# Performance work log

Measured on AMD Instinct MI355X. Metric: run time of the kernel, lower is better.

The kernel has to match this reference:

```python
import jax, jax.numpy as jnp
import numpy as np

B, A, H, L = 4096, 4096, 768, 4  # batch, num_atoms, hidden_dim, antecedent_len


def setup_inputs() -> dict:
    key = jax.random.key(0)
    ks = jax.random.split(key, 10)
    s = 0.02
    cls = jax.random.normal(ks[0], (B, H), jnp.float32)
    x_ = jax.random.bernoulli(ks[1], 0.5, (B, A)).astype(jnp.float32)
    gru_w_ih = jax.random.normal(ks[2], (3 * H, H), jnp.float32) * s
    gru_w_hh = jax.random.normal(ks[3], (3 * H, H), jnp.float32) * s
    gru_b_ih = jax.random.normal(ks[4], (3 * H,), jnp.float32) * s
    gru_b_hh = jax.random.normal(ks[5], (3 * H,), jnp.float32) * s
    head_w = jax.random.normal(ks[6], (A, H), jnp.float32) * s
    head_b = jax.random.normal(ks[7], (A,), jnp.float32) * s
    ae_weight = jax.random.normal(ks[8], (A, H), jnp.float32) * s
    return {"cls": cls, "x_": x_, "gru_w_ih": gru_w_ih, "gru_w_hh": gru_w_hh,
            "gru_b_ih": gru_b_ih, "gru_b_hh": gru_b_hh, "head_w": head_w,
            "head_b": head_b, "ae_weight": ae_weight}


def _gru_step(x, h, w_ih, w_hh, b_ih, b_hh):
    # torch GRU gate order: r, z, n
    gi = x @ w_ih.T + b_ih          # [B, 3H]
    gh = h @ w_hh.T + b_hh
    i_r, i_z, i_n = jnp.split(gi, 3, axis=-1)
    h_r, h_z, h_n = jnp.split(gh, 3, axis=-1)
    r = jax.nn.sigmoid(i_r + h_r)
    z = jax.nn.sigmoid(i_z + h_z)
    n = jnp.tanh(i_n + r * h_n)
    return (1.0 - z) * n + z * h


def reference(cls, x_, gru_w_ih, gru_w_hh, gru_b_ih, gru_b_hh, head_w, head_b, ae_weight):
    key = jax.random.key(42)
    mask = x_
    h = jnp.zeros_like(cls)
    cur_input = cls
    max_index = None
    rows = jnp.arange(B)
    probs = []
    for j in range(L):
        h = _gru_step(cur_input, h, gru_w_ih, gru_w_hh, gru_b_ih, gru_b_hh)
        out = h @ head_w.T + head_b  # [B, A]  (dropout = identity in eval)
        # filtered_softmax mask update (mutations persist across steps)
        if j == 0:
            empty = jnp.sum(mask, axis=-1) == 0.0
            mask = mask.at[:, 0].set(jnp.where(empty, 1.0, mask[:, 0]))
        else:
            mask = jnp.where((max_index == 0)[:, None], 0.0, mask)
            mask = mask.at[:, 0].set(1.0)
        logits = jnp.where(mask > 0, out, -jnp.inf)
        # hard gumbel-softmax, tau=1 (straight-through)
        key, sub = jax.random.split(key)
        g = jax.random.gumbel(sub, logits.shape, logits.dtype)
        y_soft = jax.nn.softmax(logits + g, axis=1)
        idx = jnp.argmax(y_soft, axis=1)
        y_hard = jax.nn.one_hot(idx, A, dtype=y_soft.dtype)
        prob = y_hard + y_soft - jax.lax.stop_gradient(y_soft)
        max_index = idx
        # scatter zeros at the selected atom (remove from candidate set)
        mask = mask.at[rows, idx].set(0.0)
        probs.append(prob)
        atom_wsum = prob @ jax.lax.stop_gradient(ae_weight)  # [B, H]
        cur_input = cls + atom_wsum
    return jnp.stack(probs, axis=1)  # [B, L, A]
```

## Files before the change

### kernel.cpp

```cpp
#include <hip/hip_runtime.h>
#include <cstdint>
#include <cstddef>
#include <math.h>


#define KB 4096
#define KA 4096
#define KH 768
#define KL 4

typedef __attribute__((ext_vector_type(8))) short bf16x8;
typedef __attribute__((ext_vector_type(4))) float f32x4;

__host__ __device__ inline unsigned rotl32(unsigned x, int d) {
  return (x << d) | (x >> (32 - d));
}

__host__ __device__ inline void tf2x32(unsigned k0, unsigned k1,
                                       unsigned x0, unsigned x1,
                                       unsigned& o0, unsigned& o1) {
  unsigned ks2 = k0 ^ k1 ^ 0x1BD11BDAu;
  x0 += k0; x1 += k1;
#define TF_R(r) { x0 += x1; x1 = rotl32(x1, (r)); x1 ^= x0; }
  TF_R(13) TF_R(15) TF_R(26) TF_R(6)
  x0 += k1;  x1 += ks2 + 1u;
  TF_R(17) TF_R(29) TF_R(16) TF_R(24)
  x0 += ks2; x1 += k0 + 2u;
  TF_R(13) TF_R(15) TF_R(26) TF_R(6)
  x0 += k0;  x1 += k1 + 3u;
  TF_R(17) TF_R(29) TF_R(16) TF_R(24)
  x0 += k1;  x1 += ks2 + 4u;
  TF_R(13) TF_R(15) TF_R(26) TF_R(6)
  x0 += ks2; x1 += k0 + 5u;
#undef TF_R
  o0 = x0; o1 = x1;
}

__device__ inline ushort f2bf(float f) {
  unsigned u = __float_as_uint(f);
  unsigned r = (u + 0x7fffu + ((u >> 16) & 1u)) >> 16;
  return (ushort)r;
}
__device__ inline float bf2f(ushort h) {
  return __uint_as_float(((unsigned)h) << 16);
}

__device__ inline float gumbel_at(unsigned s0, unsigned s1, unsigned ctr) {
  unsigned o0, o1;
  tf2x32(s0, s1, 0u, ctr, o0, o1);
  unsigned bits = o0 ^ o1;
  float f = __uint_as_float((bits >> 9) | 0x3f800000u) - 1.0f;
  const float TINY = 1.17549435e-38f;
  float u = fmaxf(TINY, f + TINY);
  return -logf(-logf(u));
}

#define GLDS(gp, lp) \
  __builtin_amdgcn_global_load_lds( \
      (const __attribute__((address_space(1))) void*)(gp), \
      (__attribute__((address_space(3))) void*)(lp), 16, 0, 0)

__global__ __launch_bounds__(256, 4) void gemm3_nt(
    const ushort* __restrict__ Ahi, const ushort* __restrict__ Alo,
    const ushort* __restrict__ Bhi, const ushort* __restrict__ Blo,
    float* __restrict__ C, long long ldc) {
  __shared__ ushort smem[4 * 128 * 32];
  const int tid = threadIdx.x;
  const int wave = tid >> 6;
  const int lane = tid & 63;
  const long long bm = (long long)blockIdx.y * 128;
  const long long bn = (long long)blockIdx.x * 128;
  const int wm = (wave & 1) * 64;
  const int wn = (wave >> 1) * 64;

  f32x4 acc[4][4];
#pragma unroll
  for (int i = 0; i < 4; ++i)
#pragma unroll
    for (int j = 0; j < 4; ++j) acc[i][j] = (f32x4){0.f, 0.f, 0.f, 0.f};

  const int r = lane >> 2;
  const int cs = lane & 3;
  const int csrc = cs ^ ((r & 3) ^ ((r >> 2) & 3));
  const int m15 = lane & 15;
  const int kg = (lane >> 4) & 3;
  const int slot = kg ^ ((m15 & 3) ^ ((m15 >> 2) & 3));

  for (int kt = 0; kt < 24; ++kt) {
    const int k0 = kt * 32;
#pragma unroll
    for (int s = 0; s < 2; ++s) {
      const int m0 = wave * 32 + s * 16;
      const long long arow = (bm + m0 + r) * KH + k0 + csrc * 8;
      const long long brow = (bn + m0 + r) * KH + k0 + csrc * 8;
      GLDS(Ahi + arow, &smem[0 * 4096 + m0 * 32]);
      GLDS(Alo + arow, &smem[1 * 4096 + m0 * 32]);
      GLDS(Bhi + brow, &smem[2 * 4096 + m0 * 32]);
      GLDS(Blo + brow, &smem[3 * 4096 + m0 * 32]);
    }
    __syncthreads();
    bf16x8 bh[4], bl[4];
#pragma unroll
    for (int jj = 0; jj < 4; ++jj) {
      const int n = wn + jj * 16 + m15;
      bh[jj] = *(const bf16x8*)&smem[2 * 4096 + n * 32 + slot * 8];
      bl[jj] = *(const bf16x8*)&smem[3 * 4096 + n * 32 + slot * 8];
    }
#pragma unroll
    for (int i = 0; i < 4; ++i) {
      const int m = wm + i * 16 + m15;
      bf16x8 ah = *(const bf16x8*)&smem[0 * 4096 + m * 32 + slot * 8];
      bf16x8 al = *(const bf16x8*)&smem[1 * 4096 + m * 32 + slot * 8];
#pragma unroll
      for (int jj = 0; jj < 4; ++jj) {
        acc[i][jj] = __builtin_amdgcn_mfma_f32_16x16x32_bf16(ah, bh[jj], acc[i][jj], 0, 0, 0);
        acc[i][jj] = __builtin_amdgcn_mfma_f32_16x16x32_bf16(ah, bl[jj], acc[i][jj], 0, 0, 0);
        acc[i][jj] = __builtin_amdgcn_mfma_f32_16x16x32_bf16(al, bh[jj], acc[i][jj], 0, 0, 0);
      }
    }
    __syncthreads();
  }
  const int rq = (lane >> 4) * 4;
#pragma unroll
  for (int i = 0; i < 4; ++i)
#pragma unroll
    for (int j = 0; j < 4; ++j) {
      const long long n = bn + wn + j * 16 + m15;
#pragma unroll
      for (int rg = 0; rg < 4; ++rg) {
        const long long m = bm + wm + i * 16 + rq + rg;
        C[m * ldc + n] = acc[i][j][rg];
      }
    }
}

__global__ __launch_bounds__(256, 4) void gemm_fused(
    const ushort* __restrict__ hHi, const ushort* __restrict__ hLo,
    const ushort* __restrict__ WhhHi, const ushort* __restrict__ WhhLo,
    float* __restrict__ Gh, const ushort* __restrict__ HwHi,
    const float* __restrict__ head_b, ushort* __restrict__ Vbuf, int gh_nb) {
  __shared__ ushort smem[4 * 128 * 32];
  const int tid = threadIdx.x;
  const int wave = tid >> 6;
  const int lane = tid & 63;
  const int bid = blockIdx.x;
  const int wm = (wave & 1) * 64;
  const int wn = (wave >> 1) * 64;
  const int r = lane >> 2;
  const int cs = lane & 3;
  const int csrc = cs ^ ((r & 3) ^ ((r >> 2) & 3));
  const int m15 = lane & 15;
  const int kg = (lane >> 4) & 3;
  const int slot = kg ^ ((m15 & 3) ^ ((m15 >> 2) & 3));

  f32x4 acc[4][4];
#pragma unroll
  for (int i = 0; i < 4; ++i)
#pragma unroll
    for (int j = 0; j < 4; ++j) acc[i][j] = (f32x4){0.f, 0.f, 0.f, 0.f};

  if (bid < gh_nb) {
    const long long bm = (long long)(bid / 18) * 128;
    const long long bn = (long long)(bid % 18) * 128;
    for (int kt = 0; kt < 24; ++kt) {
      const int k0 = kt * 32;
#pragma unroll
      for (int s = 0; s < 2; ++s) {
        const int m0 = wave * 32 + s * 16;
        const long long arow = (bm + m0 + r) * KH + k0 + csrc * 8;
        const long long brow = (bn + m0 + r) * KH + k0 + csrc * 8;
        GLDS(hHi + arow, &smem[0 * 4096 + m0 * 32]);
        GLDS(hLo + arow, &smem[1 * 4096 + m0 * 32]);
        GLDS(WhhHi + brow, &smem[2 * 4096 + m0 * 32]);
        GLDS(WhhLo + brow, &smem[3 * 4096 + m0 * 32]);
      }
      __syncthreads();
      bf16x8 bh[4], bl[4];
#pragma unroll
      for (int jj = 0; jj < 4; ++jj) {
        const int n = wn + jj * 16 + m15;
        bh[jj] = *(const bf16x8*)&smem[2 * 4096 + n * 32 + slot * 8];
        bl[jj] = *(const bf16x8*)&smem[3 * 4096 + n * 32 + slot * 8];
      }
#pragma unroll
      for (int i = 0; i < 4; ++i) {
        const int m = wm + i * 16 + m15;
        bf16x8 ah = *(const bf16x8*)&smem[0 * 4096 + m * 32 + slot * 8];
        bf16x8 al = *(const bf16x8*)&smem[1 * 4096 + m * 32 + slot * 8];
#pragma unroll
        for (int jj = 0; jj < 4; ++jj) {
          acc[i][jj] = __builtin_amdgcn_mfma_f32_16x16x32_bf16(ah, bh[jj], acc[i][jj], 0, 0, 0);
          acc[i][jj] = __builtin_amdgcn_mfma_f32_16x16x32_bf16(ah, bl[jj], acc[i][jj], 0, 0, 0);
          acc[i][jj] = __builtin_amdgcn_mfma_f32_16x16x32_bf16(al, bh[jj], acc[i][jj], 0, 0, 0);
        }
      }
      __syncthreads();
    }
    const int rq = (lane >> 4) * 4;
#pragma unroll
    for (int i = 0; i < 4; ++i)
#pragma unroll
      for (int j = 0; j < 4; ++j) {
        const long long n = bn + wn + j * 16 + m15;
#pragma unroll
        for (int rg = 0; rg < 4; ++rg) {
          const long long m = bm + wm + i * 16 + rq + rg;
          Gh[m * (3 * KH) + n] = acc[i][j][rg];
        }
      }
  } else {
    const int k = bid - gh_nb;
    const long long bm = (long long)(k >> 5) * 128;
    const long long bn = (long long)(k & 31) * 128;
    for (int kt = 0; kt < 24; ++kt) {
      const int k0 = kt * 32;
#pragma unroll
      for (int s = 0; s < 2; ++s) {
        const int m0 = wave * 32 + s * 16;
        const long long arow = (bm + m0 + r) * KH + k0 + csrc * 8;
        const long long brow = (bn + m0 + r) * KH + k0 + csrc * 8;
        GLDS(hHi + arow, &smem[0 * 4096 + m0 * 32]);
        GLDS(HwHi + brow, &smem[1 * 4096 + m0 * 32]);
      }
      __syncthreads();
      bf16x8 bh[4];
#pragma unroll
      for (int jj = 0; jj < 4; ++jj) {
        const int n = wn + jj * 16 + m15;
        bh[jj] = *(const bf16x8*)&smem[1 * 4096 + n * 32 + slot * 8];
      }
#pragma unroll
      for (int i = 0; i < 4; ++i) {
        const int m = wm + i * 16 + m15;
        bf16x8 ah = *(const bf16x8*)&smem[0 * 4096 + m * 32 + slot * 8];
#pragma unroll
        for (int jj = 0; jj < 4; ++jj)
          acc[i][jj] = __builtin_amdgcn_mfma_f32_16x16x32_bf16(ah, bh[jj], acc[i][jj], 0, 0, 0);
      }
      __syncthreads();
    }
    const int rq = (lane >> 4) * 4;
#pragma unroll
    for (int i = 0; i < 4; ++i)
#pragma unroll
      for (int j = 0; j < 4; ++j) {
        const long long n = bn + wn + j * 16 + m15;
        const float hb = head_b[n];
#pragma unroll
        for (int rg = 0; rg < 4; ++rg) {
          const long long m = bm + wm + i * 16 + rq + rg;
          Vbuf[m * KA + n] = f2bf(acc[i][j][rg] + hb);
        }
      }
  }
}

#define CUM1 442368
#define CUM2 884736
#define CUM3 1671168
#define CUM4 2457600
#define CUM5 3244032
#define PREP_CONV_BLOCKS 12672

__global__ void prep(const float* __restrict__ w_ih, const float* __restrict__ w_hh,
                     const float* __restrict__ head_w, const float* __restrict__ cls,
                     const float* __restrict__ ae_w, const float* __restrict__ x_,
                     ushort* __restrict__ WihHi, ushort* __restrict__ WihLo,
                     ushort* __restrict__ WhhHi, ushort* __restrict__ WhhLo,
                     ushort* __restrict__ HwHi, ushort* __restrict__ CAhi,
                     ushort* __restrict__ CAlo, unsigned char* __restrict__ empty) {
  const int blk = blockIdx.x;
  const int tid = threadIdx.x;
  if (blk < PREP_CONV_BLOCKS) {
    const int i = blk * 256 + tid;
    const float* src; ushort* dhi; ushort* dlo; int base; int split; int ofs = 0;
    if (i < CUM1)      { src = w_ih;   dhi = WihHi; dlo = WihLo; base = 0;    split = 1; }
    else if (i < CUM2) { src = w_hh;   dhi = WhhHi; dlo = WhhLo; base = CUM1; split = 1; }
    else if (i < CUM3) { src = head_w; dhi = HwHi;  dlo = 0;     base = CUM2; split = 0; }
    else if (i < CUM4) { src = cls;    dhi = CAhi;  dlo = CAlo;  base = CUM3; split = 1; }
    else               { src = ae_w;   dhi = CAhi;  dlo = CAlo;  base = CUM4; split = 1; ofs = 786432; }
    const int k = i - base;
    float4 v = ((const float4*)src)[k];
    ushort4 h;
    h.x = f2bf(v.x); h.y = f2bf(v.y); h.z = f2bf(v.z); h.w = f2bf(v.w);
    ((ushort4*)dhi)[ofs + k] = h;
    if (split) {
      ushort4 l;
      l.x = f2bf(v.x - bf2f(h.x)); l.y = f2bf(v.y - bf2f(h.y));
      l.z = f2bf(v.z - bf2f(h.z)); l.w = f2bf(v.w - bf2f(h.w));
      ((ushort4*)dlo)[ofs + k] = l;
    }
  } else {
    const int row = blk - PREP_CONV_BLOCKS;
    __shared__ int scnt[256];
    const float4* xr = (const float4*)(x_ + (size_t)row * KA);
    int cnt = 0;
#pragma unroll
    for (int k = 0; k < 4; ++k) {
      float4 v = xr[tid + (k << 8)];
      cnt += (v.x != 0.f) + (v.y != 0.f) + (v.z != 0.f) + (v.w != 0.f);
    }
    scnt[tid] = cnt;
    __syncthreads();
    for (int s = 128; s > 0; s >>= 1) {
      if (tid < s) scnt[tid] += scnt[tid + s];
      __syncthreads();
    }
    if (tid == 0) empty[row] = (scnt[0] == 0) ? 1 : 0;
  }
}

__global__ void gru_gate0(const float* __restrict__ PAE,
                          const float* __restrict__ b_ih, const float* __restrict__ b_hh,
                          float* __restrict__ h, ushort* __restrict__ hHi,
                          ushort* __restrict__ hLo) {
  int i4 = blockIdx.x * 256 + threadIdx.x;
  int b = i4 / (KH / 4);
  int c4 = i4 - b * (KH / 4);
  const f32x4* gp = (const f32x4*)(PAE + (size_t)b * (3 * KH));
  const f32x4* bi = (const f32x4*)b_ih;
  const f32x4* bhh = (const f32x4*)b_hh;
  f32x4 ir = gp[c4] + bi[c4];
  f32x4 iz = gp[c4 + 192] + bi[c4 + 192];
  f32x4 inn = gp[c4 + 384] + bi[c4 + 384];
  f32x4 hr = bhh[c4], hz = bhh[c4 + 192], hn = bhh[c4 + 384];
  f32x4 hv;
  ushort4 hh, hl;
  ushort* hhp = &hh.x;
  ushort* hlp = &hl.x;
#pragma unroll
  for (int e = 0; e < 4; ++e) {
    float rr = 1.f / (1.f + expf(-(ir[e] + hr[e])));
    float z = 1.f / (1.f + expf(-(iz[e] + hz[e])));
    float n = tanhf(inn[e] + rr * hn[e]);
    float v = (1.f - z) * n;
    hv[e] = v;
    ushort hb = f2bf(v);
    hhp[e] = hb;
    hlp[e] = f2bf(v - bf2f(hb));
  }
  ((f32x4*)h)[i4] = hv;
  ((ushort4*)hHi)[i4] = hh;
  ((ushort4*)hLo)[i4] = hl;
}

__global__ __launch_bounds__(256) void sample_gate(
    float* __restrict__ out, const ushort* __restrict__ Vbuf,
    const float* __restrict__ x_, unsigned char* __restrict__ mask,
    int* __restrict__ idxbuf, float* __restrict__ hbuf,
    const float* __restrict__ head_w, const float* __restrict__ head_b,
    const unsigned char* __restrict__ empty,
    const float* __restrict__ PAE, const float* __restrict__ Gh,
    const float* __restrict__ b_ih, const float* __restrict__ b_hh,
    ushort* __restrict__ hHi, ushort* __restrict__ hLo,
    int j, int do_gate, unsigned s0, unsigned s1) {
  const int b = blockIdx.x;
  const int tid = threadIdx.x;
  float* orow = out + ((size_t)b * KL + j) * KA;
  unsigned char* mrow = mask + (size_t)b * KA;
  const ushort* vrow = Vbuf + (size_t)b * KA;
  const float4* xrow4 = (const float4*)(x_ + (size_t)b * KA);
  __shared__ float sv[256];
  __shared__ int scand[16];
  __shared__ float srefined[16];
  __shared__ int scnt;
  __shared__ int ssel;
  const float EPS = 0.02f;

  if (tid == 0) scnt = 0;

  const int idx_prev = (j > 0) ? idxbuf[b] : 0;
  const int emp = (j == 0) ? empty[b] : 0;

  float vreg[16];
  unsigned mbits = 0;
  float lmax = -INFINITY;
#pragma unroll
  for (int k = 0; k < 2; ++k) {
    const int ci = tid + (k << 8);
    const int abase = ci * 8;
    uint4 vv = ((const uint4*)vrow)[ci];
    unsigned vw[4] = {vv.x, vv.y, vv.z, vv.w};
    float xv[8];
    unsigned mw0 = 0, mw1 = 0;
    if (j == 0) {
      float4 x0 = xrow4[ci * 2], x1 = xrow4[ci * 2 + 1];
      xv[0] = x0.x; xv[1] = x0.y; xv[2] = x0.z; xv[3] = x0.w;
      xv[4] = x1.x; xv[5] = x1.y; xv[6] = x1.z; xv[7] = x1.w;
    } else {
      uint2 mwv = ((const uint2*)mrow)[ci];
      mw0 = mwv.x; mw1 = mwv.y;
    }
#pragma unroll
    for (int e = 0; e < 8; ++e) {
      const int a = abase + e;
      int m;
      if (j == 0) {
        m = (xv[e] != 0.f) || (emp && a == 0);
      } else {
        unsigned mb = (e < 4) ? ((mw0 >> (8 * e)) & 0xffu)
                              : ((mw1 >> (8 * (e - 4))) & 0xffu);
        m = (a == 0) || (idx_prev != 0 && mb);
      }
      float v = -INFINITY;
      if (m) {
        ushort hv16 = (ushort)((vw[e >> 1] >> (16 * (e & 1))) & 0xffffu);
        float g = gumbel_at(s0, s1, (unsigned)(b * KA + a));
        v = bf2f(hv16) + g;
        mbits |= (1u << (k * 8 + e));
      }
      vreg[k * 8 + e] = v;
      lmax = fmaxf(lmax, v);
    }
  }
  sv[tid] = lmax;
  __syncthreads();
  for (int s = 128; s > 0; s >>= 1) {
    if (tid < s) sv[tid] = fmaxf(sv[tid], sv[tid + s]);
    __syncthreads();
  }
  const float vmax = sv[0];

  const float thresh = vmax - EPS;
#pragma unroll
  for (int k = 0; k < 2; ++k)
#pragma unroll
    for (int e = 0; e < 8; ++e) {
      if (vreg[k * 8 + e] >= thresh) {
        int slot = atomicAdd(&scnt, 1);
        if (slot < 16) scand[slot] = (tid + (k << 8)) * 8 + e;
      }
    }
  __syncthreads();
  const int ncand = min(scnt, 16);

  {
    const int wv = tid >> 6;
    const int lane = tid & 63;
    const float4* h4 = (const float4*)(hbuf + (size_t)b * KH);
    for (int t = wv; t < ncand; t += 4) {
      const int a = scand[t];
      const float4* w4 = (const float4*)(head_w + (size_t)a * KH);
      float sum = 0.f;
#pragma unroll
      for (int u = 0; u < 3; ++u) {
        float4 hv = h4[lane + u * 64];
        float4 wv4 = w4[lane + u * 64];
        sum = fmaf(hv.x, wv4.x, sum);
        sum = fmaf(hv.y, wv4.y, sum);
        sum = fmaf(hv.z, wv4.z, sum);
        sum = fmaf(hv.w, wv4.w, sum);
      }
#pragma unroll
      for (int off = 32; off > 0; off >>= 1) sum += __shfl_down(sum, off);
      if (lane == 0) {
        float g = gumbel_at(s0, s1, (unsigned)(b * KA + a));
        srefined[t] = sum + head_b[a] + g;
      }
    }
  }
  __syncthreads();

  if (tid == 0) {
    float best = -INFINITY;
    int bsel = KA;
    for (int t = 0; t < ncand; ++t) {
      float v = srefined[t];
      int a = scand[t];
      if (v > best || (v == best && a < bsel)) { best = v; bsel = a; }
    }
    ssel = bsel;
  }
  __syncthreads();
  const int sel = ssel;

#pragma unroll
  for (int k = 0; k < 2; ++k) {
    const int ci = tid + (k << 8);
    const int abase = ci * 8;
    unsigned mw[2] = {0u, 0u};
    float ov[8];
#pragma unroll
    for (int e = 0; e < 8; ++e) {
      const int a = abase + e;
      int m = (mbits >> (k * 8 + e)) & 1;
      if (a == sel) m = 0;
      mw[e >> 2] |= ((unsigned)m) << (8 * (e & 3));
      ov[e] = (a == sel) ? 1.f : 0.f;
    }
    ((uint2*)mrow)[ci] = make_uint2(mw[0], mw[1]);
    ((float4*)orow)[ci * 2]     = make_float4(ov[0], ov[1], ov[2], ov[3]);
    ((float4*)orow)[ci * 2 + 1] = make_float4(ov[4], ov[5], ov[6], ov[7]);
  }
  if (tid == 0) idxbuf[b] = sel;

  if (do_gate && tid < 192) {
    const int c4 = tid;
    const int i4 = b * (KH / 4) + c4;
    const f32x4* gp = (const f32x4*)(PAE + (size_t)b * (3 * KH));
    const f32x4* ga = (const f32x4*)(PAE + ((size_t)KB + sel) * (3 * KH));
    const f32x4* bi = (const f32x4*)b_ih;
    const f32x4* bhh = (const f32x4*)b_hh;
    const f32x4* gh4 = (const f32x4*)(Gh + (size_t)b * (3 * KH));
    f32x4 ir = gp[c4] + ga[c4] + bi[c4];
    f32x4 iz = gp[c4 + 192] + ga[c4 + 192] + bi[c4 + 192];
    f32x4 inn = gp[c4 + 384] + ga[c4 + 384] + bi[c4 + 384];
    f32x4 hr = bhh[c4] + gh4[c4];
    f32x4 hz = bhh[c4 + 192] + gh4[c4 + 192];
    f32x4 hn = bhh[c4 + 384] + gh4[c4 + 384];
    f32x4 hp = ((const f32x4*)hbuf)[i4];
    f32x4 hv;
    ushort4 hh, hl;
    ushort* hhp = &hh.x;
    ushort* hlp = &hl.x;
#pragma unroll
    for (int e = 0; e < 4; ++e) {
      float rr = 1.f / (1.f + expf(-(ir[e] + hr[e])));
      float z = 1.f / (1.f + expf(-(iz[e] + hz[e])));
      float n = tanhf(inn[e] + rr * hn[e]);
      float v = (1.f - z) * n + z * hp[e];
      hv[e] = v;
      ushort hb = f2bf(v);
      hhp[e] = hb;
      hlp[e] = f2bf(v - bf2f(hb));
    }
    ((f32x4*)hbuf)[i4] = hv;
    ((ushort4*)hHi)[i4] = hh;
    ((ushort4*)hLo)[i4] = hl;
  }
}

extern "C" void kernel_launch(void* const* d_in, const int* in_sizes, int n_in,
                              void* d_out, int out_size, void* d_ws, size_t ws_size,
                              hipStream_t stream) {
  const float* cls    = (const float*)d_in[0];
  const float* x_     = (const float*)d_in[1];
  const float* w_ih   = (const float*)d_in[2];
  const float* w_hh   = (const float*)d_in[3];
  const float* b_ih   = (const float*)d_in[4];
  const float* b_hh   = (const float*)d_in[5];
  const float* head_w = (const float*)d_in[6];
  const float* head_b = (const float*)d_in[7];
  const float* ae_w   = (const float*)d_in[8];
  float* out = (float*)d_out;

  char* p = (char*)d_ws;
  ushort* CAhi  = (ushort*)p; p += (size_t)2 * KB * KH * 2;
  ushort* CAlo  = (ushort*)p; p += (size_t)2 * KB * KH * 2;
  ushort* WihHi = (ushort*)p; p += (size_t)3 * KH * KH * 2;
  ushort* WihLo = (ushort*)p; p += (size_t)3 * KH * KH * 2;
  ushort* WhhHi = (ushort*)p; p += (size_t)3 * KH * KH * 2;
  ushort* WhhLo = (ushort*)p; p += (size_t)3 * KH * KH * 2;
  ushort* HwHi  = (ushort*)p; p += (size_t)KA * KH * 2;
  ushort* hHi   = (ushort*)p; p += (size_t)KB * KH * 2;
  ushort* hLo   = (ushort*)p; p += (size_t)KB * KH * 2;
  float*  hbuf  = (float*)p;  p += (size_t)KB * KH * 4;
  float*  PAE   = (float*)p;  p += (size_t)2 * KB * 3 * KH * 4;
  float*  Gh    = (float*)p;  p += (size_t)KB * 3 * KH * 4;
  ushort* Vbuf  = (ushort*)p; p += (size_t)KB * KA * 2;
  unsigned char* mask  = (unsigned char*)p; p += (size_t)KB * KA;
  unsigned char* empty = (unsigned char*)p; p += (size_t)KB;
  int* idxbuf = (int*)p; p += (size_t)KB * 4;

  unsigned key0 = 0u, key1 = 42u;
  unsigned sub0[KL], sub1[KL];
  for (int j = 0; j < KL; ++j) {
    unsigned n0, n1, t0, t1;
    tf2x32(key0, key1, 0u, 0u, n0, n1);
    tf2x32(key0, key1, 0u, 1u, t0, t1);
    sub0[j] = t0; sub1[j] = t1;
    key0 = n0; key1 = n1;
  }

  prep<<<PREP_CONV_BLOCKS + KB, 256, 0, stream>>>(
      w_ih, w_hh, head_w, cls, ae_w, x_,
      WihHi, WihLo, WhhHi, WhhLo, HwHi, CAhi, CAlo, empty);
  gemm3_nt<<<dim3(3 * KH / 128, 2 * KB / 128), 256, 0, stream>>>(
      CAhi, CAlo, WihHi, WihLo, PAE, 3 * KH);
  gru_gate0<<<KB * KH / 4 / 256, 256, 0, stream>>>(PAE, b_ih, b_hh,
                                                   hbuf, hHi, hLo);

  for (int j = 0; j < KL; ++j) {
    const int gh_nb = (j < KL - 1) ? 576 : 0;
    gemm_fused<<<gh_nb + 1024, 256, 0, stream>>>(
        hHi, hLo, WhhHi, WhhLo, Gh, HwHi, head_b, Vbuf, gh_nb);
    sample_gate<<<KB, 256, 0, stream>>>(
        out, Vbuf, x_, mask, idxbuf, hbuf, head_w, head_b, empty,
        PAE, Gh, b_ih, b_hh, hHi, hLo, j, (j < KL - 1) ? 1 : 0,
        sub0[j], sub1[j]);
  }
}
```

Measured before the change: 954.9 us.

## Precompute masked Gumbel noise in extra GEMM blocks, overlapping sampling prep

```diff
diff --git a/kernel.cpp b/kernel.cpp
--- a/kernel.cpp
+++ b/kernel.cpp
@@ -138,7 +138,9 @@
     const ushort* __restrict__ hHi, const ushort* __restrict__ hLo,
     const ushort* __restrict__ WhhHi, const ushort* __restrict__ WhhLo,
     float* __restrict__ Gh, const ushort* __restrict__ HwHi,
-    const float* __restrict__ head_b, ushort* __restrict__ Vbuf, int gh_nb) {
+    const float* __restrict__ head_b, ushort* __restrict__ Vbuf,
+    const unsigned char* __restrict__ mask, const int* __restrict__ idxbuf,
+    float* __restrict__ Gbuf, int gh_nb, int j, unsigned s0, unsigned s1) {
   __shared__ ushort smem[4 * 128 * 32];
   const int tid = threadIdx.x;
   const int wave = tid >> 6;
@@ -153,11 +155,42 @@
   const int kg = (lane >> 4) & 3;
   const int slot = kg ^ ((m15 & 3) ^ ((m15 >> 2) & 3));
 
+  if (bid >= gh_nb + 1024) {
+    const int g = bid - gh_nb - 1024;
+#pragma unroll
+    for (int rr = 0; rr < 4; ++rr) {
+      const int row = g * 4 + rr;
+      const int idx_prev = (j > 0) ? idxbuf[row] : 0;
+      const unsigned* mrow = (const unsigned*)(mask + (size_t)row * KA);
+      float4* grow = (float4*)(Gbuf + (size_t)row * KA);
+#pragma unroll
+      for (int p = 0; p < 4; ++p) {
+        const int ci = tid + (p << 8);
+        const unsigned mw = mrow[ci];
+        float4 gv;
+        float* gvp = &gv.x;
+#pragma unroll
+        for (int e = 0; e < 4; ++e) {
+          const int a = ci * 4 + e;
+          int m;
+          if (j == 0) {
+            m = (mw >> (8 * e)) & 0xffu;
+          } else {
+            m = (a == 0) || (idx_prev != 0 && ((mw >> (8 * e)) & 0xffu));
+          }
+          gvp[e] = m ? gumbel_at(s0, s1, (unsigned)(row * KA + a)) : -INFINITY;
+        }
+        grow[ci] = gv;
+      }
+    }
+    return;
+  }
+
   f32x4 acc[4][4];
 #pragma unroll
   for (int i = 0; i < 4; ++i)
 #pragma unroll
-    for (int j = 0; j < 4; ++j) acc[i][j] = (f32x4){0.f, 0.f, 0.f, 0.f};
+    for (int jj = 0; jj < 4; ++jj) acc[i][jj] = (f32x4){0.f, 0.f, 0.f, 0.f};
 
   if (bid < gh_nb) {
     const long long bm = (long long)(bid / 18) * 128;
@@ -200,12 +233,12 @@
 #pragma unroll
     for (int i = 0; i < 4; ++i)
 #pragma unroll
-      for (int j = 0; j < 4; ++j) {
-        const long long n = bn + wn + j * 16 + m15;
+      for (int jj = 0; jj < 4; ++jj) {
+        const long long n = bn + wn + jj * 16 + m15;
 #pragma unroll
         for (int rg = 0; rg < 4; ++rg) {
           const long long m = bm + wm + i * 16 + rq + rg;
-          Gh[m * (3 * KH) + n] = acc[i][j][rg];
+          Gh[m * (3 * KH) + n] = acc[i][jj][rg];
         }
       }
   } else {
@@ -243,13 +276,13 @@
 #pragma unroll
     for (int i = 0; i < 4; ++i)
 #pragma unroll
-      for (int j = 0; j < 4; ++j) {
-        const long long n = bn + wn + j * 16 + m15;
+      for (int jj = 0; jj < 4; ++jj) {
+        const long long n = bn + wn + jj * 16 + m15;
         const float hb = head_b[n];
 #pragma unroll
         for (int rg = 0; rg < 4; ++rg) {
           const long long m = bm + wm + i * 16 + rq + rg;
-          Vbuf[m * KA + n] = f2bf(acc[i][j][rg] + hb);
+          Vbuf[m * KA + n] = f2bf(acc[i][jj][rg] + hb);
         }
       }
   }
@@ -268,7 +301,7 @@
                      ushort* __restrict__ WihHi, ushort* __restrict__ WihLo,
                      ushort* __restrict__ WhhHi, ushort* __restrict__ WhhLo,
                      ushort* __restrict__ HwHi, ushort* __restrict__ CAhi,
-                     ushort* __restrict__ CAlo, unsigned char* __restrict__ empty) {
+                     ushort* __restrict__ CAlo, unsigned char* __restrict__ mask) {
   const int blk = blockIdx.x;
   const int tid = threadIdx.x;
   if (blk < PREP_CONV_BLOCKS) {
@@ -294,11 +327,12 @@
     const int row = blk - PREP_CONV_BLOCKS;
     __shared__ int scnt[256];
     const float4* xr = (const float4*)(x_ + (size_t)row * KA);
+    float4 xv[4];
     int cnt = 0;
 #pragma unroll
     for (int k = 0; k < 4; ++k) {
-      float4 v = xr[tid + (k << 8)];
-      cnt += (v.x != 0.f) + (v.y != 0.f) + (v.z != 0.f) + (v.w != 0.f);
+      xv[k] = xr[tid + (k << 8)];
+      cnt += (xv[k].x != 0.f) + (xv[k].y != 0.f) + (xv[k].z != 0.f) + (xv[k].w != 0.f);
     }
     scnt[tid] = cnt;
     __syncthreads();
@@ -306,7 +340,18 @@
       if (tid < s) scnt[tid] += scnt[tid + s];
       __syncthreads();
     }
-    if (tid == 0) empty[row] = (scnt[0] == 0) ? 1 : 0;
+    const int emp = (scnt[0] == 0);
+    unsigned* mr = (unsigned*)(mask + (size_t)row * KA);
+#pragma unroll
+    for (int k = 0; k < 4; ++k) {
+      const float* xp = &xv[k].x;
+      unsigned mw = 0;
+#pragma unroll
+      for (int e = 0; e < 4; ++e)
+        mw |= (xp[e] != 0.f) ? (1u << (8 * e)) : 0u;
+      if (emp && tid == 0 && k == 0) mw |= 1u;
+      mr[tid + (k << 8)] = mw;
+    }
   }
 }
 
@@ -346,20 +391,19 @@
 
 __global__ __launch_bounds__(256) void sample_gate(
     float* __restrict__ out, const ushort* __restrict__ Vbuf,
-    const float* __restrict__ x_, unsigned char* __restrict__ mask,
+    const float* __restrict__ Gbuf, unsigned char* __restrict__ mask,
     int* __restrict__ idxbuf, float* __restrict__ hbuf,
     const float* __restrict__ head_w, const float* __restrict__ head_b,
-    const unsigned char* __restrict__ empty,
     const float* __restrict__ PAE, const float* __restrict__ Gh,
     const float* __restrict__ b_ih, const float* __restrict__ b_hh,
     ushort* __restrict__ hHi, ushort* __restrict__ hLo,
-    int j, int do_gate, unsigned s0, unsigned s1) {
+    int j, int do_gate) {
   const int b = blockIdx.x;
   const int tid = threadIdx.x;
   float* orow = out + ((size_t)b * KL + j) * KA;
   unsigned char* mrow = mask + (size_t)b * KA;
   const ushort* vrow = Vbuf + (size_t)b * KA;
-  const float4* xrow4 = (const float4*)(x_ + (size_t)b * KA);
+  const float4* grow4 = (const float4*)(Gbuf + (size_t)b * KA);
   __shared__ float sv[256];
   __shared__ int scand[16];
   __shared__ float srefined[16];
@@ -369,46 +413,22 @@
 
   if (tid == 0) scnt = 0;
 
-  const int idx_prev = (j > 0) ? idxbuf[b] : 0;
-  const int emp = (j == 0) ? empty[b] : 0;
-
   float vreg[16];
   unsigned mbits = 0;
   float lmax = -INFINITY;
 #pragma unroll
   for (int k = 0; k < 2; ++k) {
     const int ci = tid + (k << 8);
-    const int abase = ci * 8;
     uint4 vv = ((const uint4*)vrow)[ci];
     unsigned vw[4] = {vv.x, vv.y, vv.z, vv.w};
-    float xv[8];
-    unsigned mw0 = 0, mw1 = 0;
-    if (j == 0) {
-      float4 x0 = xrow4[ci * 2], x1 = xrow4[ci * 2 + 1];
-      xv[0] = x0.x; xv[1] = x0.y; xv[2] = x0.z; xv[3] = x0.w;
-      xv[4] = x1.x; xv[5] = x1.y; xv[6] = x1.z; xv[7] = x1.w;
-    } else {
-      uint2 mwv = ((const uint2*)mrow)[ci];
-      mw0 = mwv.x; mw1 = mwv.y;
-    }
+    float4 g0 = grow4[ci * 2];
+    float4 g1 = grow4[ci * 2 + 1];
+    float gg[8] = {g0.x, g0.y, g0.z, g0.w, g1.x, g1.y, g1.z, g1.w};
 #pragma unroll
     for (int e = 0; e < 8; ++e) {
-      const int a = abase + e;
-      int m;
-      if (j == 0) {
-        m = (xv[e] != 0.f) || (emp && a == 0);
-      } else {
-        unsigned mb = (e < 4) ? ((mw0 >> (8 * e)) & 0xffu)
-                              : ((mw1 >> (8 * (e - 4))) & 0xffu);
-        m = (a == 0) || (idx_prev != 0 && mb);
-      }
-      float v = -INFINITY;
-      if (m) {
-        ushort hv16 = (ushort)((vw[e >> 1] >> (16 * (e & 1))) & 0xffffu);
-        float g = gumbel_at(s0, s1, (unsigned)(b * KA + a));
-        v = bf2f(hv16) + g;
-        mbits |= (1u << (k * 8 + e));
-      }
+      ushort hv16 = (ushort)((vw[e >> 1] >> (16 * (e & 1))) & 0xffffu);
+      float v = bf2f(hv16) + gg[e];
+      if (gg[e] != -INFINITY) mbits |= (1u << (k * 8 + e));
       vreg[k * 8 + e] = v;
       lmax = fmaxf(lmax, v);
     }
@@ -453,10 +473,8 @@
       }
 #pragma unroll
       for (int off = 32; off > 0; off >>= 1) sum += __shfl_down(sum, off);
-      if (lane == 0) {
-        float g = gumbel_at(s0, s1, (unsigned)(b * KA + a));
-        srefined[t] = sum + head_b[a] + g;
-      }
+      if (lane == 0)
+        srefined[t] = sum + head_b[a] + Gbuf[(size_t)b * KA + a];
     }
   }
   __syncthreads();
@@ -558,8 +576,8 @@
   float*  PAE   = (float*)p;  p += (size_t)2 * KB * 3 * KH * 4;
   float*  Gh    = (float*)p;  p += (size_t)KB * 3 * KH * 4;
   ushort* Vbuf  = (ushort*)p; p += (size_t)KB * KA * 2;
-  unsigned char* mask  = (unsigned char*)p; p += (size_t)KB * KA;
-  unsigned char* empty = (unsigned char*)p; p += (size_t)KB;
+  float*  Gbuf  = (float*)p;  p += (size_t)KB * KA * 4;
+  unsigned char* mask = (unsigned char*)p; p += (size_t)KB * KA;
   int* idxbuf = (int*)p; p += (size_t)KB * 4;
 
   unsigned key0 = 0u, key1 = 42u;
@@ -574,7 +592,7 @@
 
   prep<<<PREP_CONV_BLOCKS + KB, 256, 0, stream>>>(
       w_ih, w_hh, head_w, cls, ae_w, x_,
-      WihHi, WihLo, WhhHi, WhhLo, HwHi, CAhi, CAlo, empty);
+      WihHi, WihLo, WhhHi, WhhLo, HwHi, CAhi, CAlo, mask);
   gemm3_nt<<<dim3(3 * KH / 128, 2 * KB / 128), 256, 0, stream>>>(
       CAhi, CAlo, WihHi, WihLo, PAE, 3 * KH);
   gru_gate0<<<KB * KH / 4 / 256, 256, 0, stream>>>(PAE, b_ih, b_hh,
@@ -582,11 +600,11 @@
 
   for (int j = 0; j < KL; ++j) {
     const int gh_nb = (j < KL - 1) ? 576 : 0;
-    gemm_fused<<<gh_nb + 1024, 256, 0, stream>>>(
-        hHi, hLo, WhhHi, WhhLo, Gh, HwHi, head_b, Vbuf, gh_nb);
+    gemm_fused<<<gh_nb + 2048, 256, 0, stream>>>(
+        hHi, hLo, WhhHi, WhhLo, Gh, HwHi, head_b, Vbuf,
+        mask, idxbuf, Gbuf, gh_nb, j, sub0[j], sub1[j]);
     sample_gate<<<KB, 256, 0, stream>>>(
-        out, Vbuf, x_, mask, idxbuf, hbuf, head_w, head_b, empty,
-        PAE, Gh, b_ih, b_hh, hHi, hLo, j, (j < KL - 1) ? 1 : 0,
-        sub0[j], sub1[j]);
-  }
-}
+        out, Vbuf, Gbuf, mask, idxbuf, hbuf, head_w, head_b,
+        PAE, Gh, b_ih, b_hh, hHi, hLo, j, (j < KL - 1) ? 1 : 0);
+  }
+}
```

Measured after the change: 1.097 ms. 1.15x slower.

## Defer one-hot output writes into next step's GEMM launch as extra blocks

Applied to the files above, without the earlier changes.

```diff
diff --git a/kernel.cpp b/kernel.cpp
--- a/kernel.cpp
+++ b/kernel.cpp
@@ -138,12 +138,34 @@
     const ushort* __restrict__ hHi, const ushort* __restrict__ hLo,
     const ushort* __restrict__ WhhHi, const ushort* __restrict__ WhhLo,
     float* __restrict__ Gh, const ushort* __restrict__ HwHi,
-    const float* __restrict__ head_b, ushort* __restrict__ Vbuf, int gh_nb) {
+    const float* __restrict__ head_b, ushort* __restrict__ Vbuf,
+    float* __restrict__ out, const int* __restrict__ idxbuf,
+    int gh_nb, int j) {
   __shared__ ushort smem[4 * 128 * 32];
   const int tid = threadIdx.x;
   const int wave = tid >> 6;
   const int lane = tid & 63;
   const int bid = blockIdx.x;
+
+  if (bid >= gh_nb + 1024) {
+    const int w = bid - gh_nb - 1024;
+#pragma unroll 1
+    for (int rr = 0; rr < 32; ++rr) {
+      const int row = w * 32 + rr;
+      const int sel = idxbuf[row];
+      float4* orow = (float4*)(out + ((size_t)row * KL + (j - 1)) * KA);
+#pragma unroll
+      for (int p = 0; p < 4; ++p) {
+        const int ci = tid + (p << 8);
+        const int abase = ci * 4;
+        float4 v = make_float4(0.f, 0.f, 0.f, 0.f);
+        if (sel >= abase && sel < abase + 4) (&v.x)[sel - abase] = 1.f;
+        orow[ci] = v;
+      }
+    }
+    return;
+  }
+
   const int wm = (wave & 1) * 64;
   const int wn = (wave >> 1) * 64;
   const int r = lane >> 2;
@@ -157,7 +179,7 @@
 #pragma unroll
   for (int i = 0; i < 4; ++i)
 #pragma unroll
-    for (int j = 0; j < 4; ++j) acc[i][j] = (f32x4){0.f, 0.f, 0.f, 0.f};
+    for (int jj = 0; jj < 4; ++jj) acc[i][jj] = (f32x4){0.f, 0.f, 0.f, 0.f};
 
   if (bid < gh_nb) {
     const long long bm = (long long)(bid / 18) * 128;
@@ -200,12 +222,12 @@
 #pragma unroll
     for (int i = 0; i < 4; ++i)
 #pragma unroll
-      for (int j = 0; j < 4; ++j) {
-        const long long n = bn + wn + j * 16 + m15;
+      for (int jj = 0; jj < 4; ++jj) {
+        const long long n = bn + wn + jj * 16 + m15;
 #pragma unroll
         for (int rg = 0; rg < 4; ++rg) {
           const long long m = bm + wm + i * 16 + rq + rg;
-          Gh[m * (3 * KH) + n] = acc[i][j][rg];
+          Gh[m * (3 * KH) + n] = acc[i][jj][rg];
         }
       }
   } else {
@@ -243,13 +265,13 @@
 #pragma unroll
     for (int i = 0; i < 4; ++i)
 #pragma unroll
-      for (int j = 0; j < 4; ++j) {
-        const long long n = bn + wn + j * 16 + m15;
+      for (int jj = 0; jj < 4; ++jj) {
+        const long long n = bn + wn + jj * 16 + m15;
         const float hb = head_b[n];
 #pragma unroll
         for (int rg = 0; rg < 4; ++rg) {
           const long long m = bm + wm + i * 16 + rq + rg;
-          Vbuf[m * KA + n] = f2bf(acc[i][j][rg] + hb);
+          Vbuf[m * KA + n] = f2bf(acc[i][jj][rg] + hb);
         }
       }
   }
@@ -353,7 +375,7 @@
     const float* __restrict__ PAE, const float* __restrict__ Gh,
     const float* __restrict__ b_ih, const float* __restrict__ b_hh,
     ushort* __restrict__ hHi, ushort* __restrict__ hLo,
-    int j, int do_gate, unsigned s0, unsigned s1) {
+    int j, int do_gate, int write_out, unsigned s0, unsigned s1) {
   const int b = blockIdx.x;
   const int tid = threadIdx.x;
   float* orow = out + ((size_t)b * KL + j) * KA;
@@ -479,18 +501,21 @@
     const int ci = tid + (k << 8);
     const int abase = ci * 8;
     unsigned mw[2] = {0u, 0u};
-    float ov[8];
 #pragma unroll
     for (int e = 0; e < 8; ++e) {
       const int a = abase + e;
       int m = (mbits >> (k * 8 + e)) & 1;
       if (a == sel) m = 0;
       mw[e >> 2] |= ((unsigned)m) << (8 * (e & 3));
-      ov[e] = (a == sel) ? 1.f : 0.f;
     }
     ((uint2*)mrow)[ci] = make_uint2(mw[0], mw[1]);
-    ((float4*)orow)[ci * 2]     = make_float4(ov[0], ov[1], ov[2], ov[3]);
-    ((float4*)orow)[ci * 2 + 1] = make_float4(ov[4], ov[5], ov[6], ov[7]);
+    if (write_out) {
+      float ov[8];
+#pragma unroll
+      for (int e = 0; e < 8; ++e) ov[e] = (abase + e == sel) ? 1.f : 0.f;
+      ((float4*)orow)[ci * 2]     = make_float4(ov[0], ov[1], ov[2], ov[3]);
+      ((float4*)orow)[ci * 2 + 1] = make_float4(ov[4], ov[5], ov[6], ov[7]);
+    }
   }
   if (tid == 0) idxbuf[b] = sel;
 
@@ -582,11 +607,13 @@
 
   for (int j = 0; j < KL; ++j) {
     const int gh_nb = (j < KL - 1) ? 576 : 0;
-    gemm_fused<<<gh_nb + 1024, 256, 0, stream>>>(
-        hHi, hLo, WhhHi, WhhLo, Gh, HwHi, head_b, Vbuf, gh_nb);
+    const int ow_nb = (j > 0) ? 128 : 0;
+    gemm_fused<<<gh_nb + 1024 + ow_nb, 256, 0, stream>>>(
+        hHi, hLo, WhhHi, WhhLo, Gh, HwHi, head_b, Vbuf,
+        out, idxbuf, gh_nb, j);
     sample_gate<<<KB, 256, 0, stream>>>(
         out, Vbuf, x_, mask, idxbuf, hbuf, head_w, head_b, empty,
         PAE, Gh, b_ih, b_hh, hHi, hLo, j, (j < KL - 1) ? 1 : 0,
-        sub0[j], sub1[j]);
-  }
-}
+        (j == KL - 1) ? 1 : 0, sub0[j], sub1[j]);
+  }
+}
```

Result: slower. 1.067 ms (+11.7%).
